# Kernel optimization log

Measured on AMD Instinct MI355X. Metric: run time of the kernel, lower is better.

## Reference

```python
import math
import jax, jax.numpy as jnp
import numpy as np

N, T, D, H = 256, 128, 1024, 1024


def setup_inputs() -> dict:
    key = jax.random.key(0)
    k1, k2, k3, k4, k5 = jax.random.split(key, 5)
    x = jax.random.normal(k1, (N, T, D), dtype=jnp.float32)
    A = jax.random.normal(k2, (N, H, 4, 4), dtype=jnp.float32)
    Wx = jax.random.normal(k3, (D, 4 * H), dtype=jnp.float32) / math.sqrt(D)
    Wh = jax.random.normal(k4, (H, 4 * H), dtype=jnp.float32) / math.sqrt(H)
    Wattn = jax.random.normal(k5, (H, 4 * H), dtype=jnp.float32) / math.sqrt(H)
    b = jnp.zeros((4 * H,), dtype=jnp.float32)
    return {"x": x, "A": A, "Wx": Wx, "Wh": Wh, "Wattn": Wattn, "b": b}


def reference(x, A, Wx, Wh, Wattn, b):
    n, t, d = x.shape
    h = A.shape[1]
    A_flat = A.reshape(n, h, -1)            # (N, H, 16)
    h0 = A_flat.mean(axis=-1)               # mean over 4x4 grid
    c0 = h0
    scale = 1.0 / math.sqrt(h)

    def step(carry, xt):
        prev_h, prev_c = carry
        # scaled dot-product attention over the 16 spatial locations
        scores = jnp.einsum('nh,nhl->nl', prev_h, A_flat) * scale  # (N, 16)
        w = jax.nn.softmax(scores, axis=1)
        attn = jnp.einsum('nhl,nl->nh', A_flat, w)                 # (N, H)
        pre = xt @ Wx + prev_h @ Wh + attn @ Wattn + b             # (N, 4H)
        ai, af, ao, ag = jnp.split(pre, 4, axis=1)
        i = jax.nn.sigmoid(ai)
        f = jax.nn.sigmoid(af)
        o = jax.nn.sigmoid(ao)
        g = jnp.tanh(ag)
        next_c = f * prev_c + i * g
        next_h = o * jnp.tanh(next_c)
        return (next_h, next_c), next_h

    xs = jnp.swapaxes(x, 0, 1)               # (T, N, D)
    _, hs = jax.lax.scan(step, (h0, c0), xs)  # hs: (T, N, H)
    return jnp.swapaxes(hs, 0, 1)             # (N, T, H)
```

## Files before the change

kernel.cpp:

```cpp
#include <hip/hip_runtime.h>
#include <hip/hip_bf16.h>
#include <stdint.h>

#define N_ 256
#define T_ 128
#define D_ 1024
#define H_ 1024
#define FH_ 4096

typedef __bf16 bf16x8 __attribute__((ext_vector_type(8)));
typedef float f32x4 __attribute__((ext_vector_type(4)));

__global__ __launch_bounds__(256) void transpose_cast(
    const float* __restrict__ src, int cols,
    __hip_bfloat16* __restrict__ dst, int dst_stride, int dst_coloff)
{
    __shared__ float tile[32][33];
    int cb = blockIdx.x * 32, rb = blockIdx.y * 32;
    int tx = threadIdx.x, ty = threadIdx.y;
#pragma unroll
    for (int i = 0; i < 4; i++)
        tile[ty + i * 8][tx] = src[(size_t)(rb + ty + i * 8) * cols + cb + tx];
    __syncthreads();
#pragma unroll
    for (int i = 0; i < 4; i++)
        dst[(size_t)(cb + ty + i * 8) * dst_stride + dst_coloff + rb + tx] =
            __float2bfloat16(tile[tx][ty + i * 8]);
}

#define BM 64
#define BN 128
#define BK 64
#define BKP 72

__global__ __launch_bounds__(256) void gemm_x(
    const float* __restrict__ Xf,
    const __hip_bfloat16* __restrict__ BT,
    __hip_bfloat16* __restrict__ Cp, int t0)
{
    __shared__ __hip_bfloat16 Al[BM][BKP];
    __shared__ __hip_bfloat16 Bl[BN][BKP];
    const int tid = threadIdx.x;
    const int lane = tid & 63, wid = tid >> 6;
    const int m0 = blockIdx.y * BM, n0 = blockIdx.x * BN;
    const int wm = (wid >> 1) * 32, wn = (wid & 1) * 64;
    const int rs = tid >> 3, kc = (tid & 7) * 8;
    f32x4 acc[2][4] = {};

    for (int k0 = 0; k0 < D_; k0 += BK) {
#pragma unroll
        for (int p = 0; p < BM; p += 32) {
            int r = rs + p;
            int g = m0 + r;
            int nn = g & 255, tl = g >> 8;
            const float* s = Xf + ((size_t)nn * T_ + (t0 + tl)) * D_ + k0 + kc;
            float4 v0 = *reinterpret_cast<const float4*>(s);
            float4 v1 = *reinterpret_cast<const float4*>(s + 4);
            __hip_bfloat16 h8[8];
            h8[0] = __float2bfloat16(v0.x); h8[1] = __float2bfloat16(v0.y);
            h8[2] = __float2bfloat16(v0.z); h8[3] = __float2bfloat16(v0.w);
            h8[4] = __float2bfloat16(v1.x); h8[5] = __float2bfloat16(v1.y);
            h8[6] = __float2bfloat16(v1.z); h8[7] = __float2bfloat16(v1.w);
            *reinterpret_cast<int4*>(&Al[r][kc]) = *reinterpret_cast<const int4*>(h8);
        }
#pragma unroll
        for (int p = 0; p < BN; p += 32) {
            int r = rs + p;
            const __hip_bfloat16* s = BT + (size_t)(n0 + r) * D_ + k0 + kc;
            *reinterpret_cast<int4*>(&Bl[r][kc]) = *reinterpret_cast<const int4*>(s);
        }
        __syncthreads();
        const int ko = (lane >> 4) * 8;
#pragma unroll
        for (int kk = 0; kk < BK; kk += 32) {
            bf16x8 a0 = *reinterpret_cast<const bf16x8*>(&Al[wm + (lane & 15)][kk + ko]);
            bf16x8 a1 = *reinterpret_cast<const bf16x8*>(&Al[wm + 16 + (lane & 15)][kk + ko]);
#pragma unroll
            for (int ni = 0; ni < 4; ni++) {
                bf16x8 bq = *reinterpret_cast<const bf16x8*>(&Bl[wn + ni * 16 + (lane & 15)][kk + ko]);
                acc[0][ni] = __builtin_amdgcn_mfma_f32_16x16x32_bf16(a0, bq, acc[0][ni], 0, 0, 0);
                acc[1][ni] = __builtin_amdgcn_mfma_f32_16x16x32_bf16(a1, bq, acc[1][ni], 0, 0, 0);
            }
        }
        __syncthreads();
    }
    const int cr = (lane >> 4) * 4, ccol = lane & 15;
#pragma unroll
    for (int mi = 0; mi < 2; mi++)
#pragma unroll
        for (int ni = 0; ni < 4; ni++)
#pragma unroll
            for (int r = 0; r < 4; r++) {
                size_t idx = (size_t)(m0 + wm + mi * 16 + cr + r) * FH_ + (n0 + wn + ni * 16 + ccol);
                Cp[idx] = __float2bfloat16(acc[mi][ni][r]);
            }
}

__global__ __launch_bounds__(256) void aw_gemm(
    const float* __restrict__ A, const __hip_bfloat16* __restrict__ WaT,
    __hip_bfloat16* __restrict__ AW)
{
    __shared__ __hip_bfloat16 Al[16][72];
    __shared__ __hip_bfloat16 Bl[128][72];
    const int tid = threadIdx.x, lane = tid & 63, wv = tid >> 6;
    const int n = blockIdx.y, j0 = blockIdx.x * 128;
    const int rs = tid >> 3, kc = (tid & 7) * 8;
    f32x4 acc[2] = {};
    for (int k0 = 0; k0 < 1024; k0 += 64) {
        {
            int h = tid >> 2, lq = (tid & 3) * 4;
            float4 v = *reinterpret_cast<const float4*>(A + ((size_t)n * 1024 + k0 + h) * 16 + lq);
            Al[lq + 0][h] = __float2bfloat16(v.x);
            Al[lq + 1][h] = __float2bfloat16(v.y);
            Al[lq + 2][h] = __float2bfloat16(v.z);
            Al[lq + 3][h] = __float2bfloat16(v.w);
        }
#pragma unroll
        for (int p = 0; p < 128; p += 32) {
            int r = rs + p;
            *reinterpret_cast<int4*>(&Bl[r][kc]) =
                *reinterpret_cast<const int4*>(WaT + (size_t)(j0 + r) * 1024 + k0 + kc);
        }
        __syncthreads();
        const int ko = (lane >> 4) * 8;
#pragma unroll
        for (int kk = 0; kk < 64; kk += 32) {
            bf16x8 a0 = *reinterpret_cast<const bf16x8*>(&Al[lane & 15][kk + ko]);
#pragma unroll
            for (int nf = 0; nf < 2; nf++) {
                bf16x8 bq = *reinterpret_cast<const bf16x8*>(&Bl[wv * 32 + nf * 16 + (lane & 15)][kk + ko]);
                acc[nf] = __builtin_amdgcn_mfma_f32_16x16x32_bf16(a0, bq, acc[nf], 0, 0, 0);
            }
        }
        __syncthreads();
    }
    const int cr = (lane >> 4) * 4, cc = lane & 15;
#pragma unroll
    for (int nf = 0; nf < 2; nf++) {
        __hip_bfloat16 t4[4];
#pragma unroll
        for (int r = 0; r < 4; r++) t4[r] = __float2bfloat16(acc[nf][r]);
        *reinterpret_cast<uint2*>(AW + ((size_t)n * 4096 + j0 + wv * 32 + nf * 16 + cc) * 16 + cr) =
            *reinterpret_cast<uint2*>(t4);
    }
}

__global__ __launch_bounds__(256) void abf_cast(
    const float* __restrict__ A, __hip_bfloat16* __restrict__ Abf)
{
    size_t i = ((size_t)blockIdx.x * 256 + threadIdx.x) * 4;
    float4 v = *reinterpret_cast<const float4*>(A + i);
    __hip_bfloat16 o[4];
    o[0] = __float2bfloat16(v.x); o[1] = __float2bfloat16(v.y);
    o[2] = __float2bfloat16(v.z); o[3] = __float2bfloat16(v.w);
    *reinterpret_cast<uint2*>(Abf + i) = *reinterpret_cast<uint2*>(o);
}

__global__ __launch_bounds__(256) void init_s(
    const float* __restrict__ A, float* __restrict__ cbuf,
    __hip_bfloat16* __restrict__ hb0, float* __restrict__ sp0)
{
    __shared__ float red[4][16];
    const int n = blockIdx.x, tid = threadIdx.x;
    const int lane = tid & 63, wvv = tid >> 6;
    float a[4][16];
    float hv[4];
#pragma unroll
    for (int q = 0; q < 4; q++) {
        const float4* Ap = reinterpret_cast<const float4*>(A + ((size_t)n * H_ + tid * 4 + q) * 16);
        float4 q0 = Ap[0], q1 = Ap[1], q2 = Ap[2], q3 = Ap[3];
        a[q][0] = q0.x; a[q][1] = q0.y; a[q][2] = q0.z; a[q][3] = q0.w;
        a[q][4] = q1.x; a[q][5] = q1.y; a[q][6] = q1.z; a[q][7] = q1.w;
        a[q][8] = q2.x; a[q][9] = q2.y; a[q][10] = q2.z; a[q][11] = q2.w;
        a[q][12] = q3.x; a[q][13] = q3.y; a[q][14] = q3.z; a[q][15] = q3.w;
        float s = 0.f;
#pragma unroll
        for (int l = 0; l < 16; l++) s += a[q][l];
        hv[q] = s * 0.0625f;
    }
    *reinterpret_cast<float4*>(cbuf + (size_t)n * H_ + tid * 4) = *reinterpret_cast<float4*>(hv);
    __hip_bfloat16 h4[4];
#pragma unroll
    for (int q = 0; q < 4; q++) h4[q] = __float2bfloat16(hv[q]);
    *reinterpret_cast<uint2*>(hb0 + (size_t)n * H_ + tid * 4) = *reinterpret_cast<uint2*>(h4);
    float spv[16];
#pragma unroll
    for (int l = 0; l < 16; l++)
        spv[l] = hv[0] * a[0][l] + hv[1] * a[1][l] + hv[2] * a[2][l] + hv[3] * a[3][l];
#pragma unroll
    for (int l = 0; l < 16; l++) {
        spv[l] += __shfl_xor(spv[l], 1);  spv[l] += __shfl_xor(spv[l], 2);
        spv[l] += __shfl_xor(spv[l], 4);  spv[l] += __shfl_xor(spv[l], 8);
        spv[l] += __shfl_xor(spv[l], 16); spv[l] += __shfl_xor(spv[l], 32);
    }
    if (lane == 0) {
#pragma unroll
        for (int l = 0; l < 16; l++) red[wvv][l] = spv[l];
    }
    __syncthreads();
    float* spn = sp0 + (size_t)n * 1024;
    if (tid < 16)
        spn[tid] = red[0][tid] + red[1][tid] + red[2][tid] + red[3][tid];
#pragma unroll
    for (int j = 0; j < 4; j++) {
        int idx = 16 + tid * 4 + j;
        if (idx < 1024) spn[idx] = 0.f;
    }
}

#define LDAp 136

__global__ __launch_bounds__(512) void step_fused(
    const __hip_bfloat16* __restrict__ hb_in,
    __hip_bfloat16* __restrict__ hb_out,
    const __hip_bfloat16* __restrict__ WhT,
    const __hip_bfloat16* __restrict__ AW,
    const __hip_bfloat16* __restrict__ Abf,
    const __hip_bfloat16* __restrict__ xp,
    const float* __restrict__ bias,
    float* __restrict__ cbuf,
    const float* __restrict__ sp_in,
    float* __restrict__ sp_out,
    float* __restrict__ out, int t)
{
    __shared__ __align__(16) char smem[69632];
    __shared__ float wl[64][16];
    float* pls = (float*)smem;

    const int tid = threadIdx.x;
    const int lane = tid & 63, wv = tid >> 6;
    const int bid = blockIdx.x;
    const int q = bid >> 3;
    const int ct = (bid & 7) + 8 * (q >> 2);
    const int r  = q & 3;
    const int hc0 = ct * 16, n0 = r * 64;
    const int rs = tid >> 4;
    const int kc = (tid & 15) * 8;
    const int l15 = lane & 15, ko8 = (lane >> 4) * 8;
    const int wm = (wv >> 1) * 16, wn = (wv & 1) * 32;

    const int j0 = (rs >> 4) * 1024 + hc0 + (rs & 15);
    const int j1 = ((rs + 32) >> 4) * 1024 + hc0 + ((rs + 32) & 15);
    const __hip_bfloat16* aS0 = hb_in + (size_t)(n0 + rs) * H_ + kc;
    const __hip_bfloat16* aS1 = hb_in + (size_t)(n0 + rs + 32) * H_ + kc;
    const __hip_bfloat16* bS0 = WhT + (size_t)j0 * H_ + kc;
    const __hip_bfloat16* bS1 = WhT + (size_t)j1 * H_ + kc;

    int4 ra0, ra1, rb0, rb1;
    auto LOAD = [&](int k0) {
        ra0 = *reinterpret_cast<const int4*>(aS0 + k0);
        ra1 = *reinterpret_cast<const int4*>(aS1 + k0);
        rb0 = *reinterpret_cast<const int4*>(bS0 + k0);
        rb1 = *reinterpret_cast<const int4*>(bS1 + k0);
    };
    auto WRITE = [&](int b) {
        __hip_bfloat16* Al = (__hip_bfloat16*)(smem + b * 17408);
        __hip_bfloat16* Bl = (__hip_bfloat16*)(smem + 34816 + b * 17408);
        *reinterpret_cast<int4*>(Al + rs * LDAp + kc) = ra0;
        *reinterpret_cast<int4*>(Al + (rs + 32) * LDAp + kc) = ra1;
        *reinterpret_cast<int4*>(Bl + rs * LDAp + kc) = rb0;
        *reinterpret_cast<int4*>(Bl + (rs + 32) * LDAp + kc) = rb1;
    };

    {
        const int row8 = tid >> 3, l2 = (tid & 7) * 2;
        const float* spn = sp_in + (size_t)(n0 + row8) * 1024 + l2;
        float s0 = 0.f, s1 = 0.f;
#pragma unroll 8
        for (int cj = 0; cj < 64; cj++) {
            float2 v = *reinterpret_cast<const float2*>(spn + cj * 16);
            s0 += v.x; s1 += v.y;
        }
        s0 *= 0.03125f; s1 *= 0.03125f;
        float m = fmaxf(s0, s1);
        m = fmaxf(m, __shfl_xor(m, 1));
        m = fmaxf(m, __shfl_xor(m, 2));
        m = fmaxf(m, __shfl_xor(m, 4));
        float e0 = __expf(s0 - m), e1 = __expf(s1 - m);
        float se = e0 + e1;
        se += __shfl_xor(se, 1); se += __shfl_xor(se, 2); se += __shfl_xor(se, 4);
        float inv = 1.f / se;
        wl[row8][l2] = e0 * inv;
        wl[row8][l2 + 1] = e1 * inv;
    }

    LOAD(0);
    WRITE(0);
    __syncthreads();

    f32x4 acc0{}, acc1{};
#pragma unroll 1
    for (int it = 0; it < 8; ++it) {
        if (it < 7) LOAD((it + 1) * 128);
        const int cur = it & 1;
        const __hip_bfloat16* pA  = (const __hip_bfloat16*)(smem + cur * 17408) + (wm + l15) * LDAp + ko8;
        const __hip_bfloat16* pB0 = (const __hip_bfloat16*)(smem + 34816 + cur * 17408) + (wn + l15) * LDAp + ko8;
        const __hip_bfloat16* pB1 = pB0 + 16 * LDAp;
#pragma unroll
        for (int kf = 0; kf < 4; kf++) {
            bf16x8 af = *reinterpret_cast<const bf16x8*>(pA + kf * 32);
            bf16x8 b0 = *reinterpret_cast<const bf16x8*>(pB0 + kf * 32);
            bf16x8 b1 = *reinterpret_cast<const bf16x8*>(pB1 + kf * 32);
            acc0 = __builtin_amdgcn_mfma_f32_16x16x32_bf16(af, b0, acc0, 0, 0, 0);
            acc1 = __builtin_amdgcn_mfma_f32_16x16x32_bf16(af, b1, acc1, 0, 0, 0);
        }
        __syncthreads();
        if (it < 7) {
            WRITE(cur ^ 1);
            __syncthreads();
        }
    }

    {
        const int cr = (lane >> 4) * 4;
#pragma unroll
        for (int r4 = 0; r4 < 4; r4++) {
            pls[(wm + cr + r4) * 68 + wn + l15]      = acc0[r4];
            pls[(wm + cr + r4) * 68 + wn + 16 + l15] = acc1[r4];
        }
    }
    __syncthreads();

    {
        const int n_l = tid >> 3, c2 = (tid & 7) * 2;
        const int nn = n0 + n_l;
        float w[16];
#pragma unroll
        for (int l = 0; l < 16; l++) w[l] = wl[n_l][l];

        float pre[4][2];
#pragma unroll
        for (int s = 0; s < 4; s++) {
            const int gj = s * 1024 + hc0 + c2;
            __hip_bfloat16 xb[2];
            *reinterpret_cast<uint32_t*>(xb) =
                *reinterpret_cast<const uint32_t*>(xp + (size_t)nn * FH_ + gj);
            const __hip_bfloat16* awp = AW + ((size_t)nn * FH_ + gj) * 16;
#pragma unroll
            for (int cc = 0; cc < 2; cc++) {
                bf16x8 w0 = *reinterpret_cast<const bf16x8*>(awp + cc * 16);
                bf16x8 w1 = *reinterpret_cast<const bf16x8*>(awp + cc * 16 + 8);
                float aw = 0.f;
#pragma unroll
                for (int l = 0; l < 8; l++) aw += w[l] * (float)w0[l];
#pragma unroll
                for (int l = 0; l < 8; l++) aw += w[l + 8] * (float)w1[l];
                pre[s][cc] = pls[n_l * 68 + s * 16 + c2 + cc]
                           + __bfloat162float(xb[cc]) + bias[gj + cc] + aw;
            }
        }
        float hv2[2], cv2[2];
        const size_t cbase = (size_t)nn * H_ + hc0 + c2;
        float2 cold = *reinterpret_cast<const float2*>(cbuf + cbase);
        cv2[0] = cold.x; cv2[1] = cold.y;
#pragma unroll
        for (int cc = 0; cc < 2; cc++) {
            float iv = 1.f / (1.f + __expf(-pre[0][cc]));
            float fv = 1.f / (1.f + __expf(-pre[1][cc]));
            float ov = 1.f / (1.f + __expf(-pre[2][cc]));
            float gx = fminf(fmaxf(pre[3][cc], -20.f), 20.f);
            float eg = __expf(2.f * gx);
            float gv = (eg - 1.f) / (eg + 1.f);
            float c2v = fv * cv2[cc] + iv * gv;
            cv2[cc] = c2v;
            float cx = fminf(fmaxf(c2v, -20.f), 20.f);
            float ec = __expf(2.f * cx);
            hv2[cc] = ov * (ec - 1.f) / (ec + 1.f);
        }
        *reinterpret_cast<float2*>(cbuf + cbase) = make_float2(cv2[0], cv2[1]);
        *reinterpret_cast<float2*>(out + ((size_t)nn * T_ + t) * H_ + hc0 + c2) =
            make_float2(hv2[0], hv2[1]);
        __hip_bfloat16 h2[2];
        h2[0] = __float2bfloat16(hv2[0]);
        h2[1] = __float2bfloat16(hv2[1]);
        *reinterpret_cast<uint32_t*>(hb_out + (size_t)nn * H_ + hc0 + c2) =
            *reinterpret_cast<uint32_t*>(h2);

        const __hip_bfloat16* ap = Abf + ((size_t)nn * H_ + hc0 + c2) * 16;
        bf16x8 a00 = *reinterpret_cast<const bf16x8*>(ap);
        bf16x8 a01 = *reinterpret_cast<const bf16x8*>(ap + 8);
        bf16x8 a10 = *reinterpret_cast<const bf16x8*>(ap + 16);
        bf16x8 a11 = *reinterpret_cast<const bf16x8*>(ap + 24);
        float spv[16];
#pragma unroll
        for (int l = 0; l < 8; l++) {
            spv[l]     = hv2[0] * (float)a00[l] + hv2[1] * (float)a10[l];
            spv[l + 8] = hv2[0] * (float)a01[l] + hv2[1] * (float)a11[l];
        }
#pragma unroll
        for (int l = 0; l < 16; l++) {
            spv[l] += __shfl_xor(spv[l], 1);
            spv[l] += __shfl_xor(spv[l], 2);
            spv[l] += __shfl_xor(spv[l], 4);
        }
        if ((tid & 7) == 0) {
            float* d = sp_out + ((size_t)nn * 64 + ct) * 16;
            *reinterpret_cast<float4*>(d)      = *reinterpret_cast<float4*>(&spv[0]);
            *reinterpret_cast<float4*>(d + 4)  = *reinterpret_cast<float4*>(&spv[4]);
            *reinterpret_cast<float4*>(d + 8)  = *reinterpret_cast<float4*>(&spv[8]);
            *reinterpret_cast<float4*>(d + 12) = *reinterpret_cast<float4*>(&spv[12]);
        }
    }
}

extern "C" void kernel_launch(void* const* d_in, const int* in_sizes, int n_in,
                              void* d_out, int out_size, void* d_ws, size_t ws_size,
                              hipStream_t stream)
{
    const float* x     = (const float*)d_in[0];
    const float* A     = (const float*)d_in[1];
    const float* Wx    = (const float*)d_in[2];
    const float* Wh    = (const float*)d_in[3];
    const float* Wattn = (const float*)d_in[4];
    const float* b     = (const float*)d_in[5];
    float* out = (float*)d_out;
    char* ws = (char*)d_ws;
    dim3 tb(32, 8);

    const size_t SZ_WhT = (size_t)FH_ * H_ * 2;
    const size_t SZ_WxT = (size_t)FH_ * D_ * 2;
    const size_t SZ_AW  = (size_t)N_ * FH_ * 16 * 2;
    const size_t SZ_Abf = (size_t)N_ * H_ * 16 * 2;
    const size_t SZ_HB  = (size_t)N_ * H_ * 2;
    const size_t SZ_C   = (size_t)N_ * H_ * 4;
    const size_t SZ_SP  = (size_t)N_ * 64 * 16 * 4;
    const size_t SZ_XPT = (size_t)N_ * FH_ * 2;

    size_t off = 0;
    __hip_bfloat16* WhT = (__hip_bfloat16*)(ws + off); off += SZ_WhT;
    __hip_bfloat16* WxT = (__hip_bfloat16*)(ws + off); off += SZ_WxT;
    __hip_bfloat16* AW  = (__hip_bfloat16*)(ws + off); off += SZ_AW;
    __hip_bfloat16* Abf = (__hip_bfloat16*)(ws + off); off += SZ_Abf;
    __hip_bfloat16* hbA = (__hip_bfloat16*)(ws + off); off += SZ_HB;
    __hip_bfloat16* hbB = (__hip_bfloat16*)(ws + off); off += SZ_HB;
    float* cbuf = (float*)(ws + off); off += SZ_C;
    float* sp0  = (float*)(ws + off); off += SZ_SP;
    float* sp1  = (float*)(ws + off); off += SZ_SP;
    __hip_bfloat16* xpb = (__hip_bfloat16*)(ws + off);
    __hip_bfloat16* WaT = xpb;

    size_t rem = (ws_size > off) ? (ws_size - off) : 0;
    int TC = 64;
    while (TC > 1 && (size_t)TC * SZ_XPT > rem) TC >>= 1;

    transpose_cast<<<dim3(FH_ / 32, H_ / 32), tb, 0, stream>>>(Wh, FH_, WhT, H_, 0);
    transpose_cast<<<dim3(FH_ / 32, H_ / 32), tb, 0, stream>>>(Wattn, FH_, WaT, H_, 0);
    aw_gemm<<<dim3(32, N_), 256, 0, stream>>>(A, WaT, AW);
    transpose_cast<<<dim3(FH_ / 32, D_ / 32), tb, 0, stream>>>(Wx, FH_, WxT, D_, 0);
    abf_cast<<<dim3((N_ * H_ * 16) / 1024), 256, 0, stream>>>(A, Abf);
    init_s<<<N_, 256, 0, stream>>>(A, cbuf, hbA, sp0);

    __hip_bfloat16* hbp[2] = {hbA, hbB};
    float* spp[2] = {sp0, sp1};
    for (int t0 = 0; t0 < T_; t0 += TC) {
        int tc = (T_ - t0 < TC) ? (T_ - t0) : TC;
        gemm_x<<<dim3(FH_ / BN, tc * N_ / BM), 256, 0, stream>>>(x, WxT, xpb, t0);
        for (int tl = 0; tl < tc; tl++) {
            int t = t0 + tl;
            step_fused<<<dim3(256), 512, 0, stream>>>(
                hbp[t & 1], hbp[(t + 1) & 1], WhT, AW, Abf,
                xpb + (size_t)tl * N_ * FH_, b, cbuf,
                spp[t & 1], spp[(t + 1) & 1], out, t);
        }
    }
}
```

Measured before the change: 3.170 ms.

## Retile recurrent step kernel, reduce attention scores via atomics with triple buffering

The per-step kernel now launches 512 blocks of 256 threads, each covering 32 batch rows by 16 hidden columns across all four gates, in place of 256 blocks of 512 threads. The attention-score partials are now summed with atomicAdd into a compact 16-float-per-row buffer, so the next step reads one value per score instead of summing 64 partials. That buffer is triple-buffered and each step zeroes the buffer two steps ahead. Per-element operands (AW, A in bf16, x projection, bias, old cell state) are loaded before the Wh GEMM so their latency overlaps it, and the one-off AW precompute GEMM now handles 4 batch rows per block. The atomics make the float summation order nondeterministic and add contention on 16 addresses per row.

```diff
diff --git a/kernel.cpp b/kernel.cpp
--- a/kernel.cpp
+++ b/kernel.cpp
@@ -96,24 +96,28 @@
             }
 }
 
-__global__ __launch_bounds__(256) void aw_gemm(
+__global__ __launch_bounds__(256) void aw_gemm4(
     const float* __restrict__ A, const __hip_bfloat16* __restrict__ WaT,
     __hip_bfloat16* __restrict__ AW)
 {
-    __shared__ __hip_bfloat16 Al[16][72];
+    __shared__ __hip_bfloat16 Al[64][72];
     __shared__ __hip_bfloat16 Bl[128][72];
     const int tid = threadIdx.x, lane = tid & 63, wv = tid >> 6;
-    const int n = blockIdx.y, j0 = blockIdx.x * 128;
+    const int n4 = blockIdx.y * 4, j0 = blockIdx.x * 128;
     const int rs = tid >> 3, kc = (tid & 7) * 8;
-    f32x4 acc[2] = {};
+    f32x4 acc[4][2] = {};
     for (int k0 = 0; k0 < 1024; k0 += 64) {
         {
             int h = tid >> 2, lq = (tid & 3) * 4;
-            float4 v = *reinterpret_cast<const float4*>(A + ((size_t)n * 1024 + k0 + h) * 16 + lq);
-            Al[lq + 0][h] = __float2bfloat16(v.x);
-            Al[lq + 1][h] = __float2bfloat16(v.y);
-            Al[lq + 2][h] = __float2bfloat16(v.z);
-            Al[lq + 3][h] = __float2bfloat16(v.w);
+#pragma unroll
+            for (int ni = 0; ni < 4; ni++) {
+                float4 v = *reinterpret_cast<const float4*>(
+                    A + ((size_t)(n4 + ni) * 1024 + k0 + h) * 16 + lq);
+                Al[ni * 16 + lq + 0][h] = __float2bfloat16(v.x);
+                Al[ni * 16 + lq + 1][h] = __float2bfloat16(v.y);
+                Al[ni * 16 + lq + 2][h] = __float2bfloat16(v.z);
+                Al[ni * 16 + lq + 3][h] = __float2bfloat16(v.w);
+            }
         }
 #pragma unroll
         for (int p = 0; p < 128; p += 32) {
@@ -125,24 +129,32 @@
         const int ko = (lane >> 4) * 8;
 #pragma unroll
         for (int kk = 0; kk < 64; kk += 32) {
-            bf16x8 a0 = *reinterpret_cast<const bf16x8*>(&Al[lane & 15][kk + ko]);
+            bf16x8 a[4];
+#pragma unroll
+            for (int mi = 0; mi < 4; mi++)
+                a[mi] = *reinterpret_cast<const bf16x8*>(&Al[mi * 16 + (lane & 15)][kk + ko]);
 #pragma unroll
             for (int nf = 0; nf < 2; nf++) {
                 bf16x8 bq = *reinterpret_cast<const bf16x8*>(&Bl[wv * 32 + nf * 16 + (lane & 15)][kk + ko]);
-                acc[nf] = __builtin_amdgcn_mfma_f32_16x16x32_bf16(a0, bq, acc[nf], 0, 0, 0);
+#pragma unroll
+                for (int mi = 0; mi < 4; mi++)
+                    acc[mi][nf] = __builtin_amdgcn_mfma_f32_16x16x32_bf16(a[mi], bq, acc[mi][nf], 0, 0, 0);
             }
         }
         __syncthreads();
     }
     const int cr = (lane >> 4) * 4, cc = lane & 15;
 #pragma unroll
-    for (int nf = 0; nf < 2; nf++) {
-        __hip_bfloat16 t4[4];
-#pragma unroll
-        for (int r = 0; r < 4; r++) t4[r] = __float2bfloat16(acc[nf][r]);
-        *reinterpret_cast<uint2*>(AW + ((size_t)n * 4096 + j0 + wv * 32 + nf * 16 + cc) * 16 + cr) =
-            *reinterpret_cast<uint2*>(t4);
-    }
+    for (int mi = 0; mi < 4; mi++)
+#pragma unroll
+        for (int nf = 0; nf < 2; nf++) {
+            __hip_bfloat16 t4[4];
+#pragma unroll
+            for (int r = 0; r < 4; r++) t4[r] = __float2bfloat16(acc[mi][nf][r]);
+            *reinterpret_cast<uint2*>(
+                AW + ((size_t)(n4 + mi) * 4096 + j0 + wv * 32 + nf * 16 + cc) * 16 + cr) =
+                *reinterpret_cast<uint2*>(t4);
+        }
 }
 
 __global__ __launch_bounds__(256) void abf_cast(
@@ -158,7 +170,8 @@
 
 __global__ __launch_bounds__(256) void init_s(
     const float* __restrict__ A, float* __restrict__ cbuf,
-    __hip_bfloat16* __restrict__ hb0, float* __restrict__ sp0)
+    __hip_bfloat16* __restrict__ hb0, float* __restrict__ sc0,
+    float* __restrict__ sc1)
 {
     __shared__ float red[4][16];
     const int n = blockIdx.x, tid = threadIdx.x;
@@ -198,19 +211,13 @@
         for (int l = 0; l < 16; l++) red[wvv][l] = spv[l];
     }
     __syncthreads();
-    float* spn = sp0 + (size_t)n * 1024;
-    if (tid < 16)
-        spn[tid] = red[0][tid] + red[1][tid] + red[2][tid] + red[3][tid];
-#pragma unroll
-    for (int j = 0; j < 4; j++) {
-        int idx = 16 + tid * 4 + j;
-        if (idx < 1024) spn[idx] = 0.f;
-    }
-}
-
-#define LDAp 136
-
-__global__ __launch_bounds__(512) void step_fused(
+    if (tid < 16) {
+        sc0[n * 16 + tid] = red[0][tid] + red[1][tid] + red[2][tid] + red[3][tid];
+        sc1[n * 16 + tid] = 0.f;
+    }
+}
+
+__global__ __launch_bounds__(256) void step_fused(
     const __hip_bfloat16* __restrict__ hb_in,
     __hip_bfloat16* __restrict__ hb_out,
     const __hip_bfloat16* __restrict__ WhT,
@@ -219,59 +226,28 @@
     const __hip_bfloat16* __restrict__ xp,
     const float* __restrict__ bias,
     float* __restrict__ cbuf,
-    const float* __restrict__ sp_in,
-    float* __restrict__ sp_out,
+    const float* __restrict__ sc_cur,
+    float* __restrict__ sc_nxt,
+    float* __restrict__ sc_z,
     float* __restrict__ out, int t)
 {
-    __shared__ __align__(16) char smem[69632];
-    __shared__ float wl[64][16];
+    __shared__ __align__(16) char smem[54272];
+    float* wl  = (float*)(smem + 52224);
     float* pls = (float*)smem;
 
     const int tid = threadIdx.x;
     const int lane = tid & 63, wv = tid >> 6;
     const int bid = blockIdx.x;
-    const int q = bid >> 3;
-    const int ct = (bid & 7) + 8 * (q >> 2);
-    const int r  = q & 3;
-    const int hc0 = ct * 16, n0 = r * 64;
-    const int rs = tid >> 4;
-    const int kc = (tid & 15) * 8;
+    const int k = bid >> 3;
+    const int ct = (bid & 7) + 8 * (k & 7);
+    const int r = k >> 3;
+    const int hc0 = ct * 16, n0 = r * 32;
     const int l15 = lane & 15, ko8 = (lane >> 4) * 8;
-    const int wm = (wv >> 1) * 16, wn = (wv & 1) * 32;
-
-    const int j0 = (rs >> 4) * 1024 + hc0 + (rs & 15);
-    const int j1 = ((rs + 32) >> 4) * 1024 + hc0 + ((rs + 32) & 15);
-    const __hip_bfloat16* aS0 = hb_in + (size_t)(n0 + rs) * H_ + kc;
-    const __hip_bfloat16* aS1 = hb_in + (size_t)(n0 + rs + 32) * H_ + kc;
-    const __hip_bfloat16* bS0 = WhT + (size_t)j0 * H_ + kc;
-    const __hip_bfloat16* bS1 = WhT + (size_t)j1 * H_ + kc;
-
-    int4 ra0, ra1, rb0, rb1;
-    auto LOAD = [&](int k0) {
-        ra0 = *reinterpret_cast<const int4*>(aS0 + k0);
-        ra1 = *reinterpret_cast<const int4*>(aS1 + k0);
-        rb0 = *reinterpret_cast<const int4*>(bS0 + k0);
-        rb1 = *reinterpret_cast<const int4*>(bS1 + k0);
-    };
-    auto WRITE = [&](int b) {
-        __hip_bfloat16* Al = (__hip_bfloat16*)(smem + b * 17408);
-        __hip_bfloat16* Bl = (__hip_bfloat16*)(smem + 34816 + b * 17408);
-        *reinterpret_cast<int4*>(Al + rs * LDAp + kc) = ra0;
-        *reinterpret_cast<int4*>(Al + (rs + 32) * LDAp + kc) = ra1;
-        *reinterpret_cast<int4*>(Bl + rs * LDAp + kc) = rb0;
-        *reinterpret_cast<int4*>(Bl + (rs + 32) * LDAp + kc) = rb1;
-    };
 
     {
-        const int row8 = tid >> 3, l2 = (tid & 7) * 2;
-        const float* spn = sp_in + (size_t)(n0 + row8) * 1024 + l2;
-        float s0 = 0.f, s1 = 0.f;
-#pragma unroll 8
-        for (int cj = 0; cj < 64; cj++) {
-            float2 v = *reinterpret_cast<const float2*>(spn + cj * 16);
-            s0 += v.x; s1 += v.y;
-        }
-        s0 *= 0.03125f; s1 *= 0.03125f;
+        const int prow = tid >> 3, pl2 = (tid & 7) * 2;
+        float2 sv = *reinterpret_cast<const float2*>(sc_cur + (n0 + prow) * 16 + pl2);
+        float s0 = sv.x * 0.03125f, s1 = sv.y * 0.03125f;
         float m = fmaxf(s0, s1);
         m = fmaxf(m, __shfl_xor(m, 1));
         m = fmaxf(m, __shfl_xor(m, 2));
@@ -280,9 +256,68 @@
         float se = e0 + e1;
         se += __shfl_xor(se, 1); se += __shfl_xor(se, 2); se += __shfl_xor(se, 4);
         float inv = 1.f / se;
-        wl[row8][l2] = e0 * inv;
-        wl[row8][l2 + 1] = e1 * inv;
-    }
+        wl[prow * 16 + pl2] = e0 * inv;
+        wl[prow * 16 + pl2 + 1] = e1 * inv;
+    }
+    if (ct == 0) {
+        sc_z[n0 * 16 + tid * 2] = 0.f;
+        sc_z[n0 * 16 + tid * 2 + 1] = 0.f;
+    }
+
+    const int n_l = tid >> 3, c2 = (tid & 7) * 2;
+    const int nn = n0 + n_l;
+    bf16x8 awr[4][4];
+    uint32_t xr[4];
+    float2 br[4];
+#pragma unroll
+    for (int s = 0; s < 4; s++) {
+        const int gj = s * 1024 + hc0 + c2;
+        const __hip_bfloat16* awp = AW + ((size_t)nn * FH_ + gj) * 16;
+        awr[s][0] = *reinterpret_cast<const bf16x8*>(awp);
+        awr[s][1] = *reinterpret_cast<const bf16x8*>(awp + 8);
+        awr[s][2] = *reinterpret_cast<const bf16x8*>(awp + 16);
+        awr[s][3] = *reinterpret_cast<const bf16x8*>(awp + 24);
+        xr[s] = *reinterpret_cast<const uint32_t*>(xp + (size_t)nn * FH_ + gj);
+        br[s] = *reinterpret_cast<const float2*>(bias + gj);
+    }
+    bf16x8 abr[4];
+    {
+        const __hip_bfloat16* ap = Abf + ((size_t)nn * H_ + hc0 + c2) * 16;
+        abr[0] = *reinterpret_cast<const bf16x8*>(ap);
+        abr[1] = *reinterpret_cast<const bf16x8*>(ap + 8);
+        abr[2] = *reinterpret_cast<const bf16x8*>(ap + 16);
+        abr[3] = *reinterpret_cast<const bf16x8*>(ap + 24);
+    }
+    float2 cold = *reinterpret_cast<const float2*>(cbuf + (size_t)nn * H_ + hc0 + c2);
+
+    const int ar = tid >> 4;
+    const int akc = (tid & 15) * 8;
+    const __hip_bfloat16* aS0 = hb_in + (size_t)(n0 + ar) * H_ + akc;
+    const __hip_bfloat16* aS1 = hb_in + (size_t)(n0 + ar + 16) * H_ + akc;
+    const __hip_bfloat16* bS[4];
+#pragma unroll
+    for (int i = 0; i < 4; i++)
+        bS[i] = WhT + (size_t)(i * 1024 + hc0 + ar) * H_ + akc;
+
+    int4 ra0, ra1, rb0, rb1, rb2, rb3;
+    auto LOAD = [&](int k0) {
+        ra0 = *reinterpret_cast<const int4*>(aS0 + k0);
+        ra1 = *reinterpret_cast<const int4*>(aS1 + k0);
+        rb0 = *reinterpret_cast<const int4*>(bS[0] + k0);
+        rb1 = *reinterpret_cast<const int4*>(bS[1] + k0);
+        rb2 = *reinterpret_cast<const int4*>(bS[2] + k0);
+        rb3 = *reinterpret_cast<const int4*>(bS[3] + k0);
+    };
+    auto WRITE = [&](int b) {
+        __hip_bfloat16* Al = (__hip_bfloat16*)(smem + b * 8704);
+        __hip_bfloat16* Bl = (__hip_bfloat16*)(smem + 17408 + b * 17408);
+        *reinterpret_cast<int4*>(Al + ar * 136 + akc) = ra0;
+        *reinterpret_cast<int4*>(Al + (ar + 16) * 136 + akc) = ra1;
+        *reinterpret_cast<int4*>(Bl + ar * 136 + akc) = rb0;
+        *reinterpret_cast<int4*>(Bl + (ar + 16) * 136 + akc) = rb1;
+        *reinterpret_cast<int4*>(Bl + (ar + 32) * 136 + akc) = rb2;
+        *reinterpret_cast<int4*>(Bl + (ar + 48) * 136 + akc) = rb3;
+    };
 
     LOAD(0);
     WRITE(0);
@@ -293,16 +328,16 @@
     for (int it = 0; it < 8; ++it) {
         if (it < 7) LOAD((it + 1) * 128);
         const int cur = it & 1;
-        const __hip_bfloat16* pA  = (const __hip_bfloat16*)(smem + cur * 17408) + (wm + l15) * LDAp + ko8;
-        const __hip_bfloat16* pB0 = (const __hip_bfloat16*)(smem + 34816 + cur * 17408) + (wn + l15) * LDAp + ko8;
-        const __hip_bfloat16* pB1 = pB0 + 16 * LDAp;
+        const __hip_bfloat16* pA = (const __hip_bfloat16*)(smem + cur * 8704) + l15 * 136 + ko8;
+        const __hip_bfloat16* pB = (const __hip_bfloat16*)(smem + 17408 + cur * 17408)
+                                   + (wv * 16 + l15) * 136 + ko8;
 #pragma unroll
         for (int kf = 0; kf < 4; kf++) {
-            bf16x8 af = *reinterpret_cast<const bf16x8*>(pA + kf * 32);
-            bf16x8 b0 = *reinterpret_cast<const bf16x8*>(pB0 + kf * 32);
-            bf16x8 b1 = *reinterpret_cast<const bf16x8*>(pB1 + kf * 32);
-            acc0 = __builtin_amdgcn_mfma_f32_16x16x32_bf16(af, b0, acc0, 0, 0, 0);
-            acc1 = __builtin_amdgcn_mfma_f32_16x16x32_bf16(af, b1, acc1, 0, 0, 0);
+            bf16x8 a0 = *reinterpret_cast<const bf16x8*>(pA + kf * 32);
+            bf16x8 a1 = *reinterpret_cast<const bf16x8*>(pA + 16 * 136 + kf * 32);
+            bf16x8 bq = *reinterpret_cast<const bf16x8*>(pB + kf * 32);
+            acc0 = __builtin_amdgcn_mfma_f32_16x16x32_bf16(a0, bq, acc0, 0, 0, 0);
+            acc1 = __builtin_amdgcn_mfma_f32_16x16x32_bf16(a1, bq, acc1, 0, 0, 0);
         }
         __syncthreads();
         if (it < 7) {
@@ -315,44 +350,37 @@
         const int cr = (lane >> 4) * 4;
 #pragma unroll
         for (int r4 = 0; r4 < 4; r4++) {
-            pls[(wm + cr + r4) * 68 + wn + l15]      = acc0[r4];
-            pls[(wm + cr + r4) * 68 + wn + 16 + l15] = acc1[r4];
+            pls[(cr + r4) * 68 + wv * 16 + l15]      = acc0[r4];
+            pls[(16 + cr + r4) * 68 + wv * 16 + l15] = acc1[r4];
         }
     }
     __syncthreads();
 
     {
-        const int n_l = tid >> 3, c2 = (tid & 7) * 2;
-        const int nn = n0 + n_l;
         float w[16];
 #pragma unroll
-        for (int l = 0; l < 16; l++) w[l] = wl[n_l][l];
+        for (int l = 0; l < 16; l++) w[l] = wl[n_l * 16 + l];
 
         float pre[4][2];
 #pragma unroll
         for (int s = 0; s < 4; s++) {
-            const int gj = s * 1024 + hc0 + c2;
             __hip_bfloat16 xb[2];
-            *reinterpret_cast<uint32_t*>(xb) =
-                *reinterpret_cast<const uint32_t*>(xp + (size_t)nn * FH_ + gj);
-            const __hip_bfloat16* awp = AW + ((size_t)nn * FH_ + gj) * 16;
+            *reinterpret_cast<uint32_t*>(xb) = xr[s];
 #pragma unroll
             for (int cc = 0; cc < 2; cc++) {
-                bf16x8 w0 = *reinterpret_cast<const bf16x8*>(awp + cc * 16);
-                bf16x8 w1 = *reinterpret_cast<const bf16x8*>(awp + cc * 16 + 8);
+                bf16x8 w0 = awr[s][cc * 2];
+                bf16x8 w1 = awr[s][cc * 2 + 1];
                 float aw = 0.f;
 #pragma unroll
                 for (int l = 0; l < 8; l++) aw += w[l] * (float)w0[l];
 #pragma unroll
                 for (int l = 0; l < 8; l++) aw += w[l + 8] * (float)w1[l];
                 pre[s][cc] = pls[n_l * 68 + s * 16 + c2 + cc]
-                           + __bfloat162float(xb[cc]) + bias[gj + cc] + aw;
+                           + __bfloat162float(xb[cc])
+                           + (cc ? br[s].y : br[s].x) + aw;
             }
         }
-        float hv2[2], cv2[2];
-        const size_t cbase = (size_t)nn * H_ + hc0 + c2;
-        float2 cold = *reinterpret_cast<const float2*>(cbuf + cbase);
-        cv2[0] = cold.x; cv2[1] = cold.y;
+        float hv2[2], cv2[2] = {cold.x, cold.y};
 #pragma unroll
         for (int cc = 0; cc < 2; cc++) {
             float iv = 1.f / (1.f + __expf(-pre[0][cc]));
@@ -367,7 +395,8 @@
             float ec = __expf(2.f * cx);
             hv2[cc] = ov * (ec - 1.f) / (ec + 1.f);
         }
-        *reinterpret_cast<float2*>(cbuf + cbase) = make_float2(cv2[0], cv2[1]);
+        *reinterpret_cast<float2*>(cbuf + (size_t)nn * H_ + hc0 + c2) =
+            make_float2(cv2[0], cv2[1]);
         *reinterpret_cast<float2*>(out + ((size_t)nn * T_ + t) * H_ + hc0 + c2) =
             make_float2(hv2[0], hv2[1]);
         __hip_bfloat16 h2[2];
@@ -376,16 +405,11 @@
         *reinterpret_cast<uint32_t*>(hb_out + (size_t)nn * H_ + hc0 + c2) =
             *reinterpret_cast<uint32_t*>(h2);
 
-        const __hip_bfloat16* ap = Abf + ((size_t)nn * H_ + hc0 + c2) * 16;
-        bf16x8 a00 = *reinterpret_cast<const bf16x8*>(ap);
-        bf16x8 a01 = *reinterpret_cast<const bf16x8*>(ap + 8);
-        bf16x8 a10 = *reinterpret_cast<const bf16x8*>(ap + 16);
-        bf16x8 a11 = *reinterpret_cast<const bf16x8*>(ap + 24);
         float spv[16];
 #pragma unroll
         for (int l = 0; l < 8; l++) {
-            spv[l]     = hv2[0] * (float)a00[l] + hv2[1] * (float)a10[l];
-            spv[l + 8] = hv2[0] * (float)a01[l] + hv2[1] * (float)a11[l];
+            spv[l]     = hv2[0] * (float)abr[0][l] + hv2[1] * (float)abr[2][l];
+            spv[l + 8] = hv2[0] * (float)abr[1][l] + hv2[1] * (float)abr[3][l];
         }
 #pragma unroll
         for (int l = 0; l < 16; l++) {
@@ -394,11 +418,9 @@
             spv[l] += __shfl_xor(spv[l], 4);
         }
         if ((tid & 7) == 0) {
-            float* d = sp_out + ((size_t)nn * 64 + ct) * 16;
-            *reinterpret_cast<float4*>(d)      = *reinterpret_cast<float4*>(&spv[0]);
-            *reinterpret_cast<float4*>(d + 4)  = *reinterpret_cast<float4*>(&spv[4]);
-            *reinterpret_cast<float4*>(d + 8)  = *reinterpret_cast<float4*>(&spv[8]);
-            *reinterpret_cast<float4*>(d + 12) = *reinterpret_cast<float4*>(&spv[12]);
+#pragma unroll
+            for (int l = 0; l < 16; l++)
+                atomicAdd(sc_nxt + nn * 16 + l, spv[l]);
         }
     }
 }
@@ -423,7 +445,7 @@
     const size_t SZ_Abf = (size_t)N_ * H_ * 16 * 2;
     const size_t SZ_HB  = (size_t)N_ * H_ * 2;
     const size_t SZ_C   = (size_t)N_ * H_ * 4;
-    const size_t SZ_SP  = (size_t)N_ * 64 * 16 * 4;
+    const size_t SZ_SC  = 3 * (size_t)N_ * 16 * 4;
     const size_t SZ_XPT = (size_t)N_ * FH_ * 2;
 
     size_t off = 0;
@@ -434,8 +456,7 @@
     __hip_bfloat16* hbA = (__hip_bfloat16*)(ws + off); off += SZ_HB;
     __hip_bfloat16* hbB = (__hip_bfloat16*)(ws + off); off += SZ_HB;
     float* cbuf = (float*)(ws + off); off += SZ_C;
-    float* sp0  = (float*)(ws + off); off += SZ_SP;
-    float* sp1  = (float*)(ws + off); off += SZ_SP;
+    float* sc   = (float*)(ws + off); off += SZ_SC;
     __hip_bfloat16* xpb = (__hip_bfloat16*)(ws + off);
     __hip_bfloat16* WaT = xpb;
 
@@ -445,22 +466,24 @@
 
     transpose_cast<<<dim3(FH_ / 32, H_ / 32), tb, 0, stream>>>(Wh, FH_, WhT, H_, 0);
     transpose_cast<<<dim3(FH_ / 32, H_ / 32), tb, 0, stream>>>(Wattn, FH_, WaT, H_, 0);
-    aw_gemm<<<dim3(32, N_), 256, 0, stream>>>(A, WaT, AW);
+    aw_gemm4<<<dim3(32, 64), 256, 0, stream>>>(A, WaT, AW);
     transpose_cast<<<dim3(FH_ / 32, D_ / 32), tb, 0, stream>>>(Wx, FH_, WxT, D_, 0);
     abf_cast<<<dim3((N_ * H_ * 16) / 1024), 256, 0, stream>>>(A, Abf);
-    init_s<<<N_, 256, 0, stream>>>(A, cbuf, hbA, sp0);
+    init_s<<<N_, 256, 0, stream>>>(A, cbuf, hbA, sc, sc + N_ * 16);
 
     __hip_bfloat16* hbp[2] = {hbA, hbB};
-    float* spp[2] = {sp0, sp1};
     for (int t0 = 0; t0 < T_; t0 += TC) {
         int tc = (T_ - t0 < TC) ? (T_ - t0) : TC;
         gemm_x<<<dim3(FH_ / BN, tc * N_ / BM), 256, 0, stream>>>(x, WxT, xpb, t0);
         for (int tl = 0; tl < tc; tl++) {
             int t = t0 + tl;
-            step_fused<<<dim3(256), 512, 0, stream>>>(
+            step_fused<<<dim3(512), 256, 0, stream>>>(
                 hbp[t & 1], hbp[(t + 1) & 1], WhT, AW, Abf,
                 xpb + (size_t)tl * N_ * FH_, b, cbuf,
-                spp[t & 1], spp[(t + 1) & 1], out, t);
-        }
-    }
-}
+                sc + (size_t)(t % 3) * N_ * 16,
+                sc + (size_t)((t + 1) % 3) * N_ * 16,
+                sc + (size_t)((t + 2) % 3) * N_ * 16,
+                out, t);
+        }
+    }
+}
```

After: 8.153 ms. +157.2%, slower.
